# Optimization experiments

Hardware: AMD Instinct MI355X
Metric: run time of the kernel (lower is better)

The kernel has to match this reference:

```python
import jax, jax.numpy as jnp
import numpy as np

N, C, H, W = 4, 256, 60, 60
CIMG = 5  # rgb/ir channels after add_position (3 + x + y)
K = 8
ITERS = 2


def setup_inputs() -> dict:
    key = jax.random.key(0)
    ks = jax.random.split(key, 12)
    inp = {
        "cnn_encoder_output": jax.random.normal(ks[0], (N, C, H, W), jnp.float32),
        "rgb": jax.random.normal(ks[1], (N, CIMG, H, W), jnp.float32),
        "ir": jax.random.normal(ks[2], (N, CIMG, H, W), jnp.float32),
        # g-MLP (mlp_num_layers=1): Linear(2C -> C), torch weight layout [out, in]
        "W_g_rgb": jax.random.normal(ks[3], (C, 2 * C), jnp.float32) * 0.02,
        "b_g_rgb": jnp.zeros((C,), jnp.float32),
        "W_g_ir": jax.random.normal(ks[4], (C, 2 * C), jnp.float32) * 0.02,
        "b_g_ir": jnp.zeros((C,), jnp.float32),
        # SE block: Linear(2C -> C//16) -> ReLU -> Linear(C//16 -> C) -> Sigmoid
        "W_se1": jax.random.normal(ks[5], (C // 16, 2 * C), jnp.float32) * 0.02,
        "b_se1": jnp.zeros((C // 16,), jnp.float32),
        "W_se2": jax.random.normal(ks[6], (C, C // 16), jnp.float32) * 0.02,
        "b_se2": jnp.zeros((C,), jnp.float32),
        "gamma": jnp.ones((1,), jnp.float32),
        "gnn_iterations": ITERS,
        "k": K,
    }
    return inp


def _knn_indices(x, k):
    # x: [N, HW, D] -> indices of k nearest neighbours [N, HW, k]
    r = jnp.einsum("nid,njd->nij", x, x)          # gram matrix
    sq = jnp.einsum("nid,nid->ni", x, x)          # squared norms
    d2 = sq[:, :, None] + sq[:, None, :] - 2.0 * r
    d = jnp.sqrt(jnp.maximum(d2, 0.0))
    d = jax.lax.stop_gradient(d)
    _, idx = jax.lax.top_k(-d, k)                  # smallest distances
    return idx


def _gather(h, idx):
    # h: [N, HW, C], idx: [N, HW, K] -> [N, HW, K, C]
    return jax.vmap(lambda hn, i: hn[i])(h, idx)


def reference(cnn_encoder_output, rgb, ir, W_g_rgb, b_g_rgb, W_g_ir, b_g_ir,
              W_se1, b_se1, W_se2, b_se2, gamma, gnn_iterations, k):
    n, c, hh, ww = cnn_encoder_output.shape
    hw = hh * ww
    rgb_f = rgb.reshape(n, rgb.shape[1], hw).transpose(0, 2, 1)  # [N, HW, 5]
    ir_f = ir.reshape(n, ir.shape[1], hw).transpose(0, 2, 1)
    knn_rgb = _knn_indices(rgb_f, k)  # [N, HW, K]
    knn_ir = _knn_indices(ir_f, k)

    h = cnn_encoder_output.transpose(0, 2, 3, 1).reshape(n, hw, c)  # [N, HW, C]

    for _ in range(gnn_iterations):
        rgb_nb = _gather(h, knn_rgb)  # [N, HW, K, C]
        ir_nb = _gather(h, knn_ir)
        rgb_feat = jnp.concatenate([rgb_nb, rgb_nb - ir_nb], axis=-1)  # [N,HW,K,2C]
        ir_feat = jnp.concatenate([ir_nb, ir_nb - rgb_nb], axis=-1)
        m_rgb = jnp.max(jax.nn.relu(jnp.einsum("nhkf,cf->nhkc", rgb_feat, W_g_rgb) + b_g_rgb), axis=2)
        m_ir = jnp.max(jax.nn.relu(jnp.einsum("nhkf,cf->nhkc", ir_feat, W_g_ir) + b_g_ir), axis=2)
        cc = jnp.concatenate([m_rgb, m_ir], axis=-1).mean(axis=1, keepdims=True)  # [N,1,2C]
        se = jax.nn.sigmoid(jax.nn.relu(cc @ W_se1.T + b_se1) @ W_se2.T + b_se2)  # [N,1,C]
        h = se * h

    h = h.reshape(n, hh, ww, c).transpose(0, 3, 1, 2)
    return jax.nn.relu(gamma * h + cnn_encoder_output)
```

## Files before the change

kernel.cpp:

```cpp
#include <hip/hip_runtime.h>
#include <hip/hip_bf16.h>

#define NB 4
#define CH 256
#define HWT 3600
#define KNN 8
#define POSB 16
#define MPAD 3712

#define SSEGP 16
#define CAND 225
#define RROWS 512

#define GEMM_BLKS 928
#define MERGE_BLKS 458

typedef __attribute__((ext_vector_type(8))) __bf16 bf16x8;
typedef __attribute__((ext_vector_type(4))) float f32x4;
typedef __attribute__((ext_vector_type(4))) unsigned u32x4;

__device__ inline float med3f(float a, float b, float c) {
    return __builtin_amdgcn_fmed3f(a, b, c);
}

__device__ __forceinline__ void insert8(float* best, float kf) {
    best[7] = med3f(best[6], best[7], kf);
    best[6] = med3f(best[5], best[6], kf);
    best[5] = med3f(best[4], best[5], kf);
    best[4] = med3f(best[3], best[4], kf);
    best[3] = med3f(best[2], best[3], kf);
    best[2] = med3f(best[1], best[2], kf);
    best[1] = med3f(best[0], best[1], kf);
    best[0] = fminf(best[0], kf);
}


__device__ __forceinline__ void gemm_body(int lid, int n, size_t wstride,
                                          const __hip_bfloat16* __restrict__ Abf,
                                          const __hip_bfloat16* __restrict__ Wbf,
                                          __hip_bfloat16* __restrict__ Yall,
                                          char* smem) {
    char* sA = smem;
    char* sB = smem + 16384;
    int w = (lid & 7) * 29 + (lid >> 3);
    int m0 = (w >> 3) * 128;
    int o0 = (w & 7) * 128;
    int t = threadIdx.x;
    int lane = t & 63, wid = t >> 6;
    int wm = wid >> 1, wo = wid & 1;

    const __hip_bfloat16* Ab = Abf + (size_t)n * MPAD * CH;
    const __hip_bfloat16* Wb = Wbf + (size_t)n * wstride;

    f32x4 acc[4][4] = {};

    int srow = t >> 3;
    int sslot = t & 7;
    int swz = (sslot ^ (srow & 7)) << 4;
    int fr = lane & 15;
    int kg = lane >> 4;
    int p = lane & 7;

    uint4 av[4], bv[4];
    auto load_tile = [&](int ks) {
#pragma unroll
        for (int r = 0; r < 4; ++r) {
            int row = srow + 32 * r;
            av[r] = *(const uint4*)(Ab + ((size_t)(m0 + row)) * CH + ks * 64 + sslot * 8);
            bv[r] = *(const uint4*)(Wb + ((size_t)(o0 + row)) * CH + ks * 64 + sslot * 8);
        }
    };
    load_tile(0);

    for (int ks = 0; ks < 4; ++ks) {
        __syncthreads();
#pragma unroll
        for (int r = 0; r < 4; ++r) {
            int row = srow + 32 * r;
            *(uint4*)(sA + row * 128 + swz) = av[r];
            *(uint4*)(sB + row * 128 + swz) = bv[r];
        }
        __syncthreads();
        if (ks < 3) load_tile(ks + 1);
#pragma unroll
        for (int kk = 0; kk < 2; ++kk) {
            bf16x8 hf[4], wf[4];
            int slot = kk * 4 + kg;
            int inrow = (slot ^ p) << 4;
#pragma unroll
            for (int f = 0; f < 4; ++f) {
                hf[f] = *(const bf16x8*)(sA + (wm * 64 + f * 16 + fr) * 128 + inrow);
                wf[f] = *(const bf16x8*)(sB + (wo * 64 + f * 16 + fr) * 128 + inrow);
            }
#pragma unroll
            for (int fa = 0; fa < 4; ++fa)
#pragma unroll
                for (int fb = 0; fb < 4; ++fb)
                    acc[fa][fb] = __builtin_amdgcn_mfma_f32_16x16x32_bf16(
                        wf[fa], hf[fb], acc[fa][fb], 0, 0, 0);
        }
    }

    __syncthreads();
#pragma unroll
    for (int fa = 0; fa < 4; ++fa)
#pragma unroll
        for (int fb = 0; fb < 4; ++fb) {
            int ml = wm * 64 + fb * 16 + fr;
            int ob = (wo * 64 + fa * 16 + kg * 4) * 2;
            f32x4 v = acc[fa][fb];
            union { ushort4 u; __hip_bfloat16 h[4]; } pk;
            pk.h[0] = __float2bfloat16(v.x);
            pk.h[1] = __float2bfloat16(v.y);
            pk.h[2] = __float2bfloat16(v.z);
            pk.h[3] = __float2bfloat16(v.w);
            int swzb = (ob & ~15) ^ ((ml & 15) << 4);
            *(ushort4*)(smem + ml * 256 + swzb + (ob & 15)) = pk.u;
        }
    __syncthreads();
    char* Yslab = (char*)(Yall + (size_t)n * HWT * 1024) + (size_t)(o0 >> 7) * HWT * 256;
    int colb = (t & 15) * 16;
#pragma unroll
    for (int i = 0; i < 8; ++i) {
        int row = i * 16 + (t >> 4);
        int grow = m0 + row;
        if (grow < HWT) {
            u32x4 v = *(const u32x4*)(smem + row * 256 + (colb ^ ((row & 15) << 4)));
            *(u32x4*)(Yslab + (size_t)grow * 256 + colb) = v;
        }
    }
}

__device__ __forceinline__ void merge_body(int mbid,
                                           const unsigned* __restrict__ partial,
                                           int* __restrict__ knn_rgb,
                                           int* __restrict__ knn_ir,
                                           float* __restrict__ ccsum) {
    if (mbid >= 450) {
        int e = (mbid - 450) * 256 + threadIdx.x;
        if (e < NB * 512) ccsum[e] = 0.f;
        return;
    }
    int tid = mbid * 256 + threadIdx.x;
    int rid = tid >> 1, sub = tid & 1;
    int nm = rid / HWT, row = rid - nm * HWT;
    const float BIG = __uint_as_float(0x7F000000u);
    float best[8];
#pragma unroll
    for (int i = 0; i < 8; ++i) best[i] = BIG;
    for (int s = sub; s < SSEGP; s += 2) {
        const unsigned* p = partial + (((size_t)(nm * SSEGP + s)) * HWT + row) * 8;
#pragma unroll
        for (int w = 0; w < 2; ++w) {
            uint4 v = ((const uint4*)p)[w];
            unsigned vv[4] = { v.x, v.y, v.z, v.w };
#pragma unroll
            for (int e = 0; e < 4; ++e) insert8(best, __uint_as_float(vv[e]));
        }
    }
    float other[8];
#pragma unroll
    for (int i = 0; i < 8; ++i) other[i] = __shfl_xor(best[i], 1);
#pragma unroll
    for (int i = 0; i < 8; ++i) insert8(best, other[i]);
    if (sub == 0) {
        int mod = nm / NB, n = nm - mod * NB;
        int* o = (mod == 0 ? knn_rgb : knn_ir) + ((size_t)n * HWT + row) * KNN;
#pragma unroll
        for (int i = 0; i < 8; ++i) o[i] = (int)(__float_as_uint(best[i]) & 0xFFFu);
    }
}

__global__ __launch_bounds__(256) void gemm_merge(const __hip_bfloat16* __restrict__ Abf,
                                                  const __hip_bfloat16* __restrict__ Wbf,
                                                  __hip_bfloat16* __restrict__ Yall,
                                                  const unsigned* __restrict__ partial,
                                                  int* __restrict__ knn_rgb,
                                                  int* __restrict__ knn_ir,
                                                  float* __restrict__ ccsum) {
    __shared__ char smem[32768];
    int bid = blockIdx.x;
    if (bid < GEMM_BLKS) {
        gemm_body(bid % 232, bid / 232, 0, Abf, Wbf, Yall, smem);
    } else {
        merge_body(bid - GEMM_BLKS, partial, knn_rgb, knn_ir, ccsum);
    }
}

__global__ __launch_bounds__(256) void gemm_k(const __hip_bfloat16* __restrict__ Abf,
                                              const __hip_bfloat16* __restrict__ Wbf,
                                              __hip_bfloat16* __restrict__ Yall) {
    __shared__ char smem[32768];
    int gid = blockIdx.x;
    gemm_body(gid % 232, gid / 232, (size_t)1024 * CH, Abf, Wbf, Yall, smem);
}

__global__ __launch_bounds__(256) void knn_main(const float* __restrict__ xpack,
                                                unsigned* __restrict__ partial) {
    int seg = blockIdx.x, rb = blockIdx.y, nm = blockIdx.z;
    int t = threadIdx.x;
    const float* xp = xpack + (size_t)nm * HWT * 8;
    int j0 = seg * CAND;

    int r0 = rb * RROWS + t;
    int r1 = r0 + 256;
    bool act0 = (r0 < HWT);
    bool act1 = (r1 < HWT);
    int rr0 = act0 ? r0 : 0;
    int rr1 = act1 ? r1 : 0;
    float4 a0 = ((const float4*)xp)[(size_t)rr0 * 2];
    float4 b0 = ((const float4*)xp)[(size_t)rr0 * 2 + 1];
    float4 a1 = ((const float4*)xp)[(size_t)rr1 * 2];
    float4 b1 = ((const float4*)xp)[(size_t)rr1 * 2 + 1];
    float s00 = -2.f * a0.x, s01 = -2.f * a0.y, s02 = -2.f * a0.z, s03 = -2.f * a0.w;
    float s04 = -2.f * b0.x;
    float s10 = -2.f * a1.x, s11 = -2.f * a1.y, s12 = -2.f * a1.z, s13 = -2.f * a1.w;
    float s14 = -2.f * b1.x;
    float rq0 = b0.y + 1.0f, rq1 = b1.y + 1.0f;

    const float BIG = __uint_as_float(0x7F000000u);
    float bst0[8], bst1[8];
#pragma unroll
    for (int i = 0; i < 8; ++i) { bst0[i] = BIG; bst1[i] = BIG; }

    const float* cp = xp + (size_t)j0 * 8;
    unsigned jg0 = (unsigned)j0;
#pragma unroll 5
    for (int jj = 0; jj < CAND; ++jj) {
        float c0 = cp[0], c1 = cp[1], c2 = cp[2], c3 = cp[3], c4 = cp[4], cq = cp[5];
        cp += 8;
        unsigned jg = jg0 + jj;
        float d0 = fmaf(c0, s00, rq0);
        d0 = fmaf(c1, s01, d0);
        d0 = fmaf(c2, s02, d0);
        d0 = fmaf(c3, s03, d0);
        d0 = fmaf(c4, s04, d0);
        float e0 = d0 + cq;
        float d1 = fmaf(c0, s10, rq1);
        d1 = fmaf(c1, s11, d1);
        d1 = fmaf(c2, s12, d1);
        d1 = fmaf(c3, s13, d1);
        d1 = fmaf(c4, s14, d1);
        float e1 = d1 + cq;
        float k0 = __uint_as_float((__float_as_uint(e0) & 0xFFFFF000u) | jg);
        float k1 = __uint_as_float((__float_as_uint(e1) & 0xFFFFF000u) | jg);
        insert8(bst0, k0);
        insert8(bst1, k1);
    }
    if (act0) {
        unsigned* o = partial + (((size_t)(nm * SSEGP + seg)) * HWT + r0) * 8;
        ((uint4*)o)[0] = uint4{ __float_as_uint(bst0[0]), __float_as_uint(bst0[1]),
                                __float_as_uint(bst0[2]), __float_as_uint(bst0[3]) };
        ((uint4*)o)[1] = uint4{ __float_as_uint(bst0[4]), __float_as_uint(bst0[5]),
                                __float_as_uint(bst0[6]), __float_as_uint(bst0[7]) };
    }
    if (act1) {
        unsigned* o1 = partial + (((size_t)(nm * SSEGP + seg)) * HWT + r1) * 8;
        ((uint4*)o1)[0] = uint4{ __float_as_uint(bst1[0]), __float_as_uint(bst1[1]),
                                 __float_as_uint(bst1[2]), __float_as_uint(bst1[3]) };
        ((uint4*)o1)[1] = uint4{ __float_as_uint(bst1[4]), __float_as_uint(bst1[5]),
                                 __float_as_uint(bst1[6]), __float_as_uint(bst1[7]) };
    }
}

__global__ __launch_bounds__(256) void fusedA(const float* __restrict__ cnn,
                                              __hip_bfloat16* __restrict__ Abf,
                                              const float* __restrict__ Wg_rgb,
                                              const float* __restrict__ Wg_ir,
                                              float* __restrict__ Wcomb,
                                              float* __restrict__ g,
                                              __hip_bfloat16* __restrict__ Wbf,
                                              const float* __restrict__ rgb,
                                              const float* __restrict__ ir,
                                              float* __restrict__ xpack) {
    int bid = blockIdx.x;
    int t = threadIdx.x;
    if (bid < GEMM_BLKS) {
        __shared__ float st[64][65];
        int n = bid / 232;
        int rem = bid - n * 232;
        int k0 = (rem / 58) * 64;
        int m0 = (rem % 58) * 64;
        const float* src = cnn + (size_t)n * CH * HWT;
#pragma unroll
        for (int r = 0; r < 4; ++r) {
            int kl = r * 16 + (t >> 4);
            int ms = (t & 15) * 4;
            float4 v = {0.f, 0.f, 0.f, 0.f};
            if (m0 + ms < HWT) v = *(const float4*)(src + (size_t)(k0 + kl) * HWT + m0 + ms);
            st[ms + 0][kl] = v.x; st[ms + 1][kl] = v.y;
            st[ms + 2][kl] = v.z; st[ms + 3][kl] = v.w;
        }
        __syncthreads();
        int m = t >> 2, kg = (t & 3) * 16;
        union { uint4 u[2]; __hip_bfloat16 h[16]; } pk;
#pragma unroll
        for (int i = 0; i < 16; ++i) pk.h[i] = __float2bfloat16(st[m][kg + i]);
        __hip_bfloat16* dst = Abf + ((size_t)n * MPAD + m0 + m) * CH + k0 + kg;
        ((uint4*)dst)[0] = pk.u[0];
        ((uint4*)dst)[1] = pk.u[1];
    } else if (bid < GEMM_BLKS + 1024) {
        int e = (bid - GEMM_BLKS) * 256 + t;
        int o = e >> 8, j = e & 255;
        float v;
        if (o < 256)      v = Wg_rgb[o * 512 + j] + Wg_rgb[o * 512 + 256 + j];
        else if (o < 512) v = Wg_rgb[(o - 256) * 512 + 256 + j];
        else if (o < 768) v = Wg_ir[(o - 512) * 512 + j] + Wg_ir[(o - 512) * 512 + 256 + j];
        else              v = Wg_ir[(o - 768) * 512 + 256 + j];
        Wcomb[e] = v;
        Wbf[e] = __float2bfloat16(v);
        if (e < NB * CH) g[e] = 1.0f;
    } else {
        int e = (bid - GEMM_BLKS - 1024) * 256 + t;
        if (e < 2 * NB * HWT) {
            int nm = e / HWT, j = e - nm * HWT;
            int mod = nm / NB, n = nm - mod * NB;
            const float* x = (mod == 0 ? rgb : ir) + (size_t)n * 5 * HWT;
            float v[5], q = 0.f;
#pragma unroll
            for (int d = 0; d < 5; ++d) { v[d] = x[d * HWT + j]; q = fmaf(v[d], v[d], q); }
            float* o = xpack + (size_t)e * 8;
#pragma unroll
            for (int d = 0; d < 5; ++d) o[d] = v[d];
            o[5] = q; o[6] = 0.f; o[7] = 0.f;
        }
    }
}

__global__ __launch_bounds__(256) void scale_w_zero(const float* __restrict__ Wcomb,
                                                    const float* __restrict__ g,
                                                    __hip_bfloat16* __restrict__ Wbf,
                                                    float* __restrict__ ccsum) {
    int bid = blockIdx.x;
    if (bid >= 512) {
        int e = (bid - 512) * 256 + threadIdx.x;
        if (e < NB * 512) ccsum[e] = 0.f;
        return;
    }
    int n = bid >> 7;
    int gid = (bid & 127) * 256 + threadIdx.x;
    int o = gid >> 5;
    int kb = (gid & 31) * 8;
    const float* w = Wcomb + o * 256 + kb;
    const float* gp = g + n * CH + kb;
    union { uint4 u; __hip_bfloat16 h[8]; } pk;
#pragma unroll
    for (int i = 0; i < 8; ++i) pk.h[i] = __float2bfloat16(w[i] * gp[i]);
    *(uint4*)(Wbf + ((size_t)n * 1024 + o) * CH + kb) = pk.u;
}

__global__ __launch_bounds__(256) void gather_kernel(const __hip_bfloat16* __restrict__ Yall,
                                                     const int* __restrict__ knn_rgb,
                                                     const int* __restrict__ knn_ir,
                                                     const float* __restrict__ b_rgb,
                                                     const float* __restrict__ b_ir,
                                                     float* __restrict__ ccsum) {
    int lid = blockIdx.x;
    int grp = lid & 15, sub = lid >> 4;
    int n = ((grp >> 3) & 1) | (((grp >> 2) & 1) << 1);
    int mod = (grp >> 1) & 1;
    int chalf = grp & 1;
    int hwbase = sub * 16;
    int t = threadIdx.x;
    int psub = t >> 6;
    int pr = t & 63;
    int cp = chalf * 128 + pr * 2;
    __shared__ int sidx[16][2][KNN];
    __shared__ float red[4][64][2];
    {
        int p = t >> 4, rem = t & 15;
        int hw = hwbase + p;
        int v;
        if (rem < 8) v = knn_rgb[((size_t)n * HWT + hw) * KNN + rem];
        else         v = knn_ir[((size_t)n * HWT + hw) * KNN + (rem - 8)];
        sidx[p][rem >> 3][rem & 7] = v;
    }
    __syncthreads();
    const float* bias = mod ? b_ir : b_rgb;
    float b0 = bias[cp], b1 = bias[cp + 1];
    float acc0 = 0.f, acc1 = 0.f;
    const char* Yn = (const char*)(Yall + (size_t)n * HWT * 1024);
    const char* YA = Yn + (size_t)(mod * 4 + chalf) * HWT * 256 + pr * 4;
    const char* YB = Yn + (size_t)(mod * 4 + 2 + chalf) * HWT * 256 + pr * 4;
    for (int p = psub * 4; p < psub * 4 + 4; ++p) {
        float m0 = 0.f, m1 = 0.f;
#pragma unroll
        for (int k = 0; k < KNN; ++k) {
            int jA = sidx[p][mod][k];
            int jB = sidx[p][mod ^ 1][k];
            unsigned u1 = *(const unsigned*)(YA + (size_t)jA * 256);
            unsigned u2 = *(const unsigned*)(YB + (size_t)jB * 256);
            float a0 = __uint_as_float(u1 << 16);
            float a1 = __uint_as_float(u1 & 0xFFFF0000u);
            float c0 = __uint_as_float(u2 << 16);
            float c1 = __uint_as_float(u2 & 0xFFFF0000u);
            m0 = fmaxf(m0, a0 - c0 + b0);
            m1 = fmaxf(m1, a1 - c1 + b1);
        }
        acc0 += m0;
        acc1 += m1;
    }
    if (psub) { red[psub][pr][0] = acc0; red[psub][pr][1] = acc1; }
    __syncthreads();
    if (psub == 0) {
#pragma unroll
        for (int q = 1; q < 4; ++q) {
            acc0 += red[q][pr][0];
            acc1 += red[q][pr][1];
        }
        atomicAdd(&ccsum[n * 512 + mod * 256 + cp], acc0);
        atomicAdd(&ccsum[n * 512 + mod * 256 + cp + 1], acc1);
    }
}

__global__ __launch_bounds__(256) void se_kernel(const float* __restrict__ ccsum,
                                                 const float* __restrict__ W1,
                                                 const float* __restrict__ b1,
                                                 const float* __restrict__ W2,
                                                 const float* __restrict__ b2,
                                                 float* __restrict__ g) {
    int n = blockIdx.x;
    int t = threadIdx.x;
    __shared__ float hid[16];
    __shared__ float cc[512];
    cc[t] = ccsum[n * 512 + t] * (1.0f / HWT);
    cc[256 + t] = ccsum[n * 512 + 256 + t] * (1.0f / HWT);
    __syncthreads();
    if (t < 16) {
        float s = b1[t];
        for (int j = 0; j < 512; ++j) s = fmaf(W1[t * 512 + j], cc[j], s);
        hid[t] = fmaxf(s, 0.f);
    }
    __syncthreads();
    float s = b2[t];
#pragma unroll
    for (int q = 0; q < 16; ++q) s = fmaf(W2[t * 16 + q], hid[q], s);
    float se = 1.0f / (1.0f + expf(-s));
    g[n * CH + t] *= se;
}

__global__ void final_kernel(const float* __restrict__ cnn, const float* __restrict__ g,
                             const float* __restrict__ gamma, float* __restrict__ out) {
    int t = blockIdx.x * blockDim.x + threadIdx.x;
    if (t >= NB * CH * HWT / 4) return;
    int nc = (t * 4) / HWT;
    float4 x = ((const float4*)cnn)[t];
    float s = gamma[0] * g[nc] + 1.0f;
    float4 o;
    o.x = fmaxf(s * x.x, 0.f);
    o.y = fmaxf(s * x.y, 0.f);
    o.z = fmaxf(s * x.z, 0.f);
    o.w = fmaxf(s * x.w, 0.f);
    ((float4*)out)[t] = o;
}

extern "C" void kernel_launch(void* const* d_in, const int* in_sizes, int n_in,
                              void* d_out, int out_size, void* d_ws, size_t ws_size,
                              hipStream_t stream) {
    const float* cnn    = (const float*)d_in[0];
    const float* rgb    = (const float*)d_in[1];
    const float* ir     = (const float*)d_in[2];
    const float* Wg_rgb = (const float*)d_in[3];
    const float* bg_rgb = (const float*)d_in[4];
    const float* Wg_ir  = (const float*)d_in[5];
    const float* bg_ir  = (const float*)d_in[6];
    const float* Wse1   = (const float*)d_in[7];
    const float* bse1   = (const float*)d_in[8];
    const float* Wse2   = (const float*)d_in[9];
    const float* bse2   = (const float*)d_in[10];
    const float* gamma  = (const float*)d_in[11];
    float* out = (float*)d_out;

    char* ws = (char*)d_ws;
    size_t off = 0;
    float* xpack = (float*)(ws + off); off += (size_t)2 * NB * HWT * 8 * 4;
    int* knn_rgb = (int*)(ws + off); off += (size_t)NB * HWT * KNN * 4;
    int* knn_ir  = (int*)(ws + off); off += (size_t)NB * HWT * KNN * 4;
    float* Wcomb = (float*)(ws + off); off += (size_t)1024 * 256 * 4;
    __hip_bfloat16* Wbf = (__hip_bfloat16*)(ws + off); off += (size_t)NB * 1024 * CH * 2;
    __hip_bfloat16* Abf = (__hip_bfloat16*)(ws + off); off += (size_t)NB * MPAD * CH * 2;
    __hip_bfloat16* Yall = (__hip_bfloat16*)(ws + off); off += (size_t)NB * HWT * 1024 * 2;
    unsigned* partial = (unsigned*)(ws + off);
    off += (size_t)2 * NB * SSEGP * HWT * 8 * 4;
    float* ccsum = (float*)(ws + off); off += (size_t)NB * 512 * 4;
    float* g     = (float*)(ws + off); off += (size_t)NB * CH * 4;

    fusedA<<<GEMM_BLKS + 1024 + 113, 256, 0, stream>>>(cnn, Abf, Wg_rgb, Wg_ir, Wcomb, g,
                                                       Wbf, rgb, ir, xpack);
    knn_main<<<dim3(SSEGP, 8, 2 * NB), 256, 0, stream>>>(xpack, partial);
    gemm_merge<<<GEMM_BLKS + MERGE_BLKS, 256, 0, stream>>>(Abf, Wbf, Yall, partial,
                                                           knn_rgb, knn_ir, ccsum);
    gather_kernel<<<3600, 256, 0, stream>>>(Yall, knn_rgb, knn_ir, bg_rgb, bg_ir, ccsum);
    se_kernel<<<NB, 256, 0, stream>>>(ccsum, Wse1, bse1, Wse2, bse2, g);
    scale_w_zero<<<520, 256, 0, stream>>>(Wcomb, g, Wbf, ccsum);
    gemm_k<<<GEMM_BLKS, 256, 0, stream>>>(Abf, Wbf, Yall);
    gather_kernel<<<3600, 256, 0, stream>>>(Yall, knn_rgb, knn_ir, bg_rgb, bg_ir, ccsum);
    se_kernel<<<NB, 256, 0, stream>>>(ccsum, Wse1, bse1, Wse2, bse2, g);
    final_kernel<<<3600, 256, 0, stream>>>(cnn, g, gamma, out);
}
```

Before: 203.0 us.

## Co-schedule first GEMM with KNN search in one launch, split merge out

Result: no change. 206.2 us (+1.6%).

```diff
diff --git a/kernel.cpp b/kernel.cpp
--- a/kernel.cpp
+++ b/kernel.cpp
@@ -5,7 +5,6 @@
 #define CH 256
 #define HWT 3600
 #define KNN 8
-#define POSB 16
 #define MPAD 3712
 
 #define SSEGP 16
@@ -13,7 +12,7 @@
 #define RROWS 512
 
 #define GEMM_BLKS 928
-#define MERGE_BLKS 458
+#define FB2_BLKS 1952
 
 typedef __attribute__((ext_vector_type(8))) __bf16 bf16x8;
 typedef __attribute__((ext_vector_type(4))) float f32x4;
@@ -35,14 +34,13 @@
 }
 
 
-__device__ __forceinline__ void gemm_body(int lid, int n, size_t wstride,
+__device__ __forceinline__ void gemm_body(int w, int n, size_t wstride,
                                           const __hip_bfloat16* __restrict__ Abf,
                                           const __hip_bfloat16* __restrict__ Wbf,
                                           __hip_bfloat16* __restrict__ Yall,
                                           char* smem) {
     char* sA = smem;
     char* sB = smem + 16384;
-    int w = (lid & 7) * 29 + (lid >> 3);
     int m0 = (w >> 3) * 128;
     int o0 = (w & 7) * 128;
     int t = threadIdx.x;
@@ -131,73 +129,11 @@
     }
 }
 
-__device__ __forceinline__ void merge_body(int mbid,
-                                           const unsigned* __restrict__ partial,
-                                           int* __restrict__ knn_rgb,
-                                           int* __restrict__ knn_ir,
-                                           float* __restrict__ ccsum) {
-    if (mbid >= 450) {
-        int e = (mbid - 450) * 256 + threadIdx.x;
-        if (e < NB * 512) ccsum[e] = 0.f;
-        return;
-    }
-    int tid = mbid * 256 + threadIdx.x;
-    int rid = tid >> 1, sub = tid & 1;
-    int nm = rid / HWT, row = rid - nm * HWT;
-    const float BIG = __uint_as_float(0x7F000000u);
-    float best[8];
-#pragma unroll
-    for (int i = 0; i < 8; ++i) best[i] = BIG;
-    for (int s = sub; s < SSEGP; s += 2) {
-        const unsigned* p = partial + (((size_t)(nm * SSEGP + s)) * HWT + row) * 8;
-#pragma unroll
-        for (int w = 0; w < 2; ++w) {
-            uint4 v = ((const uint4*)p)[w];
-            unsigned vv[4] = { v.x, v.y, v.z, v.w };
-#pragma unroll
-            for (int e = 0; e < 4; ++e) insert8(best, __uint_as_float(vv[e]));
-        }
-    }
-    float other[8];
-#pragma unroll
-    for (int i = 0; i < 8; ++i) other[i] = __shfl_xor(best[i], 1);
-#pragma unroll
-    for (int i = 0; i < 8; ++i) insert8(best, other[i]);
-    if (sub == 0) {
-        int mod = nm / NB, n = nm - mod * NB;
-        int* o = (mod == 0 ? knn_rgb : knn_ir) + ((size_t)n * HWT + row) * KNN;
-#pragma unroll
-        for (int i = 0; i < 8; ++i) o[i] = (int)(__float_as_uint(best[i]) & 0xFFFu);
-    }
-}
-
-__global__ __launch_bounds__(256) void gemm_merge(const __hip_bfloat16* __restrict__ Abf,
-                                                  const __hip_bfloat16* __restrict__ Wbf,
-                                                  __hip_bfloat16* __restrict__ Yall,
-                                                  const unsigned* __restrict__ partial,
-                                                  int* __restrict__ knn_rgb,
-                                                  int* __restrict__ knn_ir,
-                                                  float* __restrict__ ccsum) {
-    __shared__ char smem[32768];
-    int bid = blockIdx.x;
-    if (bid < GEMM_BLKS) {
-        gemm_body(bid % 232, bid / 232, 0, Abf, Wbf, Yall, smem);
-    } else {
-        merge_body(bid - GEMM_BLKS, partial, knn_rgb, knn_ir, ccsum);
-    }
-}
-
-__global__ __launch_bounds__(256) void gemm_k(const __hip_bfloat16* __restrict__ Abf,
-                                              const __hip_bfloat16* __restrict__ Wbf,
-                                              __hip_bfloat16* __restrict__ Yall) {
-    __shared__ char smem[32768];
-    int gid = blockIdx.x;
-    gemm_body(gid % 232, gid / 232, (size_t)1024 * CH, Abf, Wbf, Yall, smem);
-}
-
-__global__ __launch_bounds__(256) void knn_main(const float* __restrict__ xpack,
-                                                unsigned* __restrict__ partial) {
-    int seg = blockIdx.x, rb = blockIdx.y, nm = blockIdx.z;
+__device__ __forceinline__ void knn_body(int kid, const float* __restrict__ xpack,
+                                         unsigned* __restrict__ partial) {
+    int seg = kid & 15;
+    int rb = (kid >> 4) & 7;
+    int nm = kid >> 7;
     int t = threadIdx.x;
     const float* xp = xpack + (size_t)nm * HWT * 8;
     int j0 = seg * CAND;
@@ -260,6 +196,76 @@
                                  __float_as_uint(bst1[2]), __float_as_uint(bst1[3]) };
         ((uint4*)o1)[1] = uint4{ __float_as_uint(bst1[4]), __float_as_uint(bst1[5]),
                                  __float_as_uint(bst1[6]), __float_as_uint(bst1[7]) };
+    }
+}
+
+__global__ __launch_bounds__(256) void fusedB2(const __hip_bfloat16* __restrict__ Abf,
+                                               const __hip_bfloat16* __restrict__ Wbf,
+                                               __hip_bfloat16* __restrict__ Yall,
+                                               const float* __restrict__ xpack,
+                                               unsigned* __restrict__ partial) {
+    __shared__ char smem[32768];
+    int bid = blockIdx.x;
+    if (bid < 1856 && !(bid & 1)) {
+        int gid = bid >> 1;
+        int n = gid / 232;
+        int l = gid - n * 232;
+        int w = (l & 3) * 58 + (l >> 2);
+        gemm_body(w, n, 0, Abf, Wbf, Yall, smem);
+    } else {
+        int kid = (bid < 1856) ? (bid >> 1) : (928 + bid - 1856);
+        knn_body(kid, xpack, partial);
+    }
+}
+
+__global__ __launch_bounds__(256) void gemm_k(const __hip_bfloat16* __restrict__ Abf,
+                                              const __hip_bfloat16* __restrict__ Wbf,
+                                              __hip_bfloat16* __restrict__ Yall) {
+    __shared__ char smem[32768];
+    int gid = blockIdx.x;
+    int n = gid / 232;
+    int l = gid - n * 232;
+    int w = (l & 7) * 29 + (l >> 3);
+    gemm_body(w, n, (size_t)1024 * CH, Abf, Wbf, Yall, smem);
+}
+
+__global__ __launch_bounds__(256) void knn_merge_zero(const unsigned* __restrict__ partial,
+                                                      int* __restrict__ knn_rgb,
+                                                      int* __restrict__ knn_ir,
+                                                      float* __restrict__ ccsum) {
+    int bid = blockIdx.x;
+    if (bid >= 450) {
+        int e = (bid - 450) * 256 + threadIdx.x;
+        if (e < NB * 512) ccsum[e] = 0.f;
+        return;
+    }
+    int tid = bid * 256 + threadIdx.x;
+    int rid = tid >> 1, sub = tid & 1;
+    int nm = rid / HWT, row = rid - nm * HWT;
+    const float BIG = __uint_as_float(0x7F000000u);
+    float best[8];
+#pragma unroll
+    for (int i = 0; i < 8; ++i) best[i] = BIG;
+    for (int s = sub; s < SSEGP; s += 2) {
+        const unsigned* p = partial + (((size_t)(nm * SSEGP + s)) * HWT + row) * 8;
+#pragma unroll
+        for (int w = 0; w < 2; ++w) {
+            uint4 v = ((const uint4*)p)[w];
+            unsigned vv[4] = { v.x, v.y, v.z, v.w };
+#pragma unroll
+            for (int e = 0; e < 4; ++e) insert8(best, __uint_as_float(vv[e]));
+        }
+    }
+    float other[8];
+#pragma unroll
+    for (int i = 0; i < 8; ++i) other[i] = __shfl_xor(best[i], 1);
+#pragma unroll
+    for (int i = 0; i < 8; ++i) insert8(best, other[i]);
+    if (sub == 0) {
+        int mod = nm / NB, n = nm - mod * NB;
+        int* o = (mod == 0 ? knn_rgb : knn_ir) + ((size_t)n * HWT + row) * KNN;
+#pragma unroll
+        for (int i = 0; i < 8; ++i) o[i] = (int)(__float_as_uint(best[i]) & 0xFFFu);
     }
 }
 
@@ -487,9 +493,8 @@
 
     fusedA<<<GEMM_BLKS + 1024 + 113, 256, 0, stream>>>(cnn, Abf, Wg_rgb, Wg_ir, Wcomb, g,
                                                        Wbf, rgb, ir, xpack);
-    knn_main<<<dim3(SSEGP, 8, 2 * NB), 256, 0, stream>>>(xpack, partial);
-    gemm_merge<<<GEMM_BLKS + MERGE_BLKS, 256, 0, stream>>>(Abf, Wbf, Yall, partial,
-                                                           knn_rgb, knn_ir, ccsum);
+    fusedB2<<<FB2_BLKS, 256, 0, stream>>>(Abf, Wbf, Yall, xpack, partial);
+    knn_merge_zero<<<458, 256, 0, stream>>>(partial, knn_rgb, knn_ir, ccsum);
     gather_kernel<<<3600, 256, 0, stream>>>(Yall, knn_rgb, knn_ir, bg_rgb, bg_ir, ccsum);
     se_kernel<<<NB, 256, 0, stream>>>(ccsum, Wse1, bse1, Wse2, bse2, g);
     scale_w_zero<<<520, 256, 0, stream>>>(Wcomb, g, Wbf, ccsum);
```
